# Kernel optimization log

Measured on AMD Instinct MI355X. Metric: run time of the kernel, lower is better.

Reference implementation:

```python
import jax, jax.numpy as jnp
import numpy as np

N_WAY = 2
K_SHOT = 5
C = 320
NPTS = 2048
NQ = 2
K_PROTO = 100  # hardcoded k=100 in forward
N_CLS = N_WAY + 1
SIGMA = 1.0
NEG = -1e9


def _l2norm(x, eps=1e-8):
    return x / (jnp.linalg.norm(x, axis=-1, keepdims=True) + eps)


def _class_prototypes(feat, mask, k):
    """Multi-prototype masked pooling for one class.
    feat: [M, C] point features; mask: [M] float (1 = belongs to class).
    Picks k masked seed points, assigns every masked point to its
    nearest (cosine) seed, and returns the k masked cluster means.
    """
    M = feat.shape[0]
    # deterministic seeds: first k masked points (tie-break by index)
    score = mask - jnp.arange(M, dtype=feat.dtype) * 1e-9
    _, seed_idx = jax.lax.top_k(score, k)
    seeds = feat[seed_idx]                      # [k, C]
    sim = _l2norm(feat) @ _l2norm(seeds).T      # [M, k]
    assign = jnp.argmax(sim, axis=1)            # [M]
    onehot = jax.nn.one_hot(assign, k, dtype=feat.dtype) * mask[:, None]  # [M, k]
    num = onehot.T @ feat                       # [k, C]
    den = onehot.sum(axis=0)[:, None] + 1e-8
    return num / den


def _fg_prototypes(support_feat, fg_mask, k):
    # support_feat [n_way, k_shot, C, N] -> per-class point sets [n_way, k_shot*N, C]
    feat = support_feat.transpose(0, 1, 3, 2).reshape(N_WAY, -1, C)
    m = fg_mask.reshape(N_WAY, -1).astype(feat.dtype)
    protos = jax.vmap(lambda f, mm: _class_prototypes(f, mm, k))(feat, m)  # [n_way, k, C]
    labels = jnp.repeat(jnp.arange(1, N_WAY + 1), k)                        # classes 1..n_way
    return protos.reshape(-1, C), jax.nn.one_hot(labels, N_CLS, dtype=feat.dtype)


def _bg_prototypes(support_feat, bg_mask, k):
    feat = support_feat.transpose(0, 1, 3, 2).reshape(-1, C)   # all shots pooled
    m = bg_mask.reshape(-1).astype(feat.dtype)
    protos = _class_prototypes(feat, m, k)                      # [k, C]
    labels = jnp.zeros((k,), dtype=jnp.int32)                   # class 0 = background
    return protos, jax.nn.one_hot(labels, N_CLS, dtype=feat.dtype)


def _predict(prototypes, proto_onehot, qfeat, qlabels):
    # cosine similarity [M, P], per-class max over that class's prototypes
    sim = (_l2norm(qfeat) @ _l2norm(prototypes).T) / SIGMA        # [M, P]
    cls_mask = proto_onehot.T[None] > 0                            # [1, ncls, P]
    pred = jnp.max(jnp.where(cls_mask, sim[:, None, :], NEG), axis=-1)  # [M, ncls]
    logp = jax.nn.log_softmax(pred, axis=-1)
    loss = -jnp.mean(jnp.take_along_axis(logp, qlabels.reshape(-1, 1), axis=1))
    query_pred = pred.reshape(NQ, NPTS, N_CLS).transpose(0, 2, 1)  # [NQ, ncls, NPTS]
    return loss, query_pred


def reference(support_feat, query_feat, support_y, query_y):
    fg_mask = support_y
    bg_mask = 1 - support_y
    fg_protos, fg_labels = _fg_prototypes(support_feat, fg_mask, K_PROTO)
    bg_protos, bg_labels = _bg_prototypes(support_feat, bg_mask, K_PROTO)
    prototypes = jnp.concatenate([bg_protos, fg_protos], axis=0)           # [P, C]
    proto_labels = jnp.concatenate([bg_labels, fg_labels], axis=0)         # [P, ncls]

    qfeat = query_feat.transpose(0, 2, 1).reshape(-1, C)                   # [NQ*NPTS, C]
    loss, query_pred = _predict(prototypes, proto_labels, qfeat, query_y)
    # the forward adds computeCrossEntropyLoss(query_pred, query_y): same CE again
    loss = loss * 2.0

    # post-hoc per-point confidence thresholding (vectorized Python loop)
    qp = jnp.concatenate([query_pred[0], query_pred[1]], axis=-1)          # [ncls, NQ*NPTS]
    predictions = jnp.argmax(qp, axis=0)
    confidences = jnp.max(qp, axis=0)
    final = jnp.where(confidences > jnp.mean(confidences), predictions, -1)
    final_labels = jnp.stack([final[:NPTS], final[NPTS:]], axis=0)         # [2, NPTS]
    return loss, query_pred, final_labels


def setup_inputs() -> dict:
    key = jax.random.key(0)
    k1, k2, k3, k4 = jax.random.split(key, 4)
    return {
        "support_feat": jax.random.normal(k1, (N_WAY, K_SHOT, C, NPTS), dtype=jnp.float32),
        "query_feat": jax.random.normal(k2, (NQ, C, NPTS), dtype=jnp.float32),
        "support_y": jax.random.randint(k3, (N_WAY, K_SHOT, NPTS), 0, 2, dtype=jnp.int32),
        "query_y": jax.random.randint(k4, (NQ, NPTS), 0, 3, dtype=jnp.int32),
    }
```

## Files before the change

### kernel.cpp

```cpp
#include <hip/hip_runtime.h>
#include <math.h>

#define C 320
#define NPTS 2048
#define SUPPTS 20480
#define QPTS 4096
#define KP 100
#define NCLS 3
#define PSTRIDE 300

__global__ __launch_bounds__(64) void k_protoseed(const float* __restrict__ sup,
                                                  const int* __restrict__ sy,
                                                  float* __restrict__ pbufT) {
    int p    = blockIdx.x;
    int lane = threadIdx.x;
    int prob = (p < 100) ? 2 : ((p < 200) ? 0 : 1);
    int rank = (p < 100) ? p : ((p < 200) ? p - 100 : p - 200);
    int M    = (prob == 2) ? SUPPTS : 10240;
    int base = (prob == 1) ? 10240 : 0;
    int found = 0, sp = 0;
    for (int chunk = 0; chunk < M; chunk += 64) {
        int yy = sy[base + chunk + lane];
        int m  = (prob == 2) ? (1 - yy) : yy;
        unsigned long long bal = __ballot(m != 0);
        int cnt = __popcll(bal);
        if (found + cnt > rank) {
            int need = rank - found;
            int prefix = __popcll(bal & ((1ull << lane) - 1ull));
            unsigned long long match = __ballot(m && (prefix == need));
            int pos = __ffsll((unsigned long long)match) - 1;
            sp = base + chunk + pos;
            break;
        }
        found += cnt;
    }
    const float* fb = sup + ((size_t)(sp >> 11) * C) * NPTS + (sp & 2047);
    float v[5]; float s = 0.f;
    #pragma unroll
    for (int i = 0; i < 5; i++) {
        v[i] = fb[(size_t)(lane + i * 64) * NPTS];
        s += v[i] * v[i];
    }
    #pragma unroll
    for (int off = 32; off > 0; off >>= 1) s += __shfl_down(s, off);
    s = __shfl(s, 0);
    float r = 1.0f / (sqrtf(s) + 1e-8f);
    #pragma unroll
    for (int i = 0; i < 5; i++)
        pbufT[(size_t)(lane + i * 64) * PSTRIDE + p] = v[i] * r;
}

__global__ __launch_bounds__(128) void k_assign(const float* __restrict__ sup,
                                                const float* __restrict__ pbT,
                                                float* __restrict__ pmaxv,
                                                int* __restrict__ pmaxj) {
    __shared__ float shp[C * 20];
    int b = blockIdx.x, jt = blockIdx.y, tid = threadIdx.x;
    int prob, pt, gbase, aoff;
    if (b < 40)       { prob = 0; pt = b * 256;         gbase = 0;     aoff = 0; }
    else if (b < 80)  { prob = 1; pt = (b - 40) * 256;  gbase = 10240; aoff = 10240; }
    else              { prob = 2; pt = (b - 80) * 256;  gbase = 0;     aoff = 20480; }
    int j0 = jt * 20;
    int col0 = (prob == 2) ? 0 : (100 + prob * 100);
    for (int i = tid; i < C * 20; i += 128) {
        int j = i % 20, c = i / 20;
        shp[i] = pbT[(size_t)c * PSTRIDE + col0 + j0 + j];
    }
    __syncthreads();
    int g = gbase + pt + tid * 2;
    const float* fb = sup + ((size_t)(g >> 11) * C) * NPTS + (g & 2047);
    float acc0[20], acc1[20];
    #pragma unroll
    for (int j = 0; j < 20; j++) { acc0[j] = 0.f; acc1[j] = 0.f; }
    float2 pf[8];
    #pragma unroll
    for (int k = 0; k < 8; k++) pf[k] = *(const float2*)(fb + (size_t)k * NPTS);
    for (int cc = 0; cc < C; cc += 8) {
        float2 cur[8];
        #pragma unroll
        for (int k = 0; k < 8; k++) cur[k] = pf[k];
        if (cc + 8 < C) {
            #pragma unroll
            for (int k = 0; k < 8; k++) pf[k] = *(const float2*)(fb + (size_t)(cc + 8 + k) * NPTS);
        }
        #pragma unroll
        for (int k = 0; k < 8; k++) {
            const float4* r = (const float4*)&shp[(cc + k) * 20];
            float4 a = r[0], d1 = r[1], d2 = r[2], d3 = r[3], d4 = r[4];
            float px = cur[k].x, py = cur[k].y;
            acc0[0]+=px*a.x;  acc1[0]+=py*a.x;  acc0[1]+=px*a.y;  acc1[1]+=py*a.y;
            acc0[2]+=px*a.z;  acc1[2]+=py*a.z;  acc0[3]+=px*a.w;  acc1[3]+=py*a.w;
            acc0[4]+=px*d1.x; acc1[4]+=py*d1.x; acc0[5]+=px*d1.y; acc1[5]+=py*d1.y;
            acc0[6]+=px*d1.z; acc1[6]+=py*d1.z; acc0[7]+=px*d1.w; acc1[7]+=py*d1.w;
            acc0[8]+=px*d2.x; acc1[8]+=py*d2.x; acc0[9]+=px*d2.y; acc1[9]+=py*d2.y;
            acc0[10]+=px*d2.z;acc1[10]+=py*d2.z;acc0[11]+=px*d2.w;acc1[11]+=py*d2.w;
            acc0[12]+=px*d3.x;acc1[12]+=py*d3.x;acc0[13]+=px*d3.y;acc1[13]+=py*d3.y;
            acc0[14]+=px*d3.z;acc1[14]+=py*d3.z;acc0[15]+=px*d3.w;acc1[15]+=py*d3.w;
            acc0[16]+=px*d4.x;acc1[16]+=py*d4.x;acc0[17]+=px*d4.y;acc1[17]+=py*d4.y;
            acc0[18]+=px*d4.z;acc1[18]+=py*d4.z;acc0[19]+=px*d4.w;acc1[19]+=py*d4.w;
        }
    }
    float bv0 = acc0[0]; int bj0 = 0;
    float bv1 = acc1[0]; int bj1 = 0;
    #pragma unroll
    for (int j = 1; j < 20; j++) {
        if (acc0[j] > bv0) { bv0 = acc0[j]; bj0 = j; }
        if (acc1[j] > bv1) { bv1 = acc1[j]; bj1 = j; }
    }
    size_t a0 = (size_t)jt * 40960 + (aoff + pt + tid * 2);
    pmaxv[a0]     = bv0; pmaxj[a0]     = j0 + bj0;
    pmaxv[a0 + 1] = bv1; pmaxj[a0 + 1] = j0 + bj1;
}

__global__ __launch_bounds__(256) void k_combine_dst(const float* __restrict__ pmaxv,
                                                     const int* __restrict__ pmaxj,
                                                     const int* __restrict__ sy,
                                                     int* __restrict__ dst,
                                                     float* __restrict__ loss) {
    int g = blockIdx.x * 256 + threadIdx.x;
    if (g == 0) loss[0] = 0.f;
    if (g == 1) loss[1] = 0.f;
    float bvf = pmaxv[g]; int bjf = pmaxj[g];
    #pragma unroll
    for (int t = 1; t < 5; t++) {
        float v = pmaxv[(size_t)t * 40960 + g];
        if (v > bvf) { bvf = v; bjf = pmaxj[(size_t)t * 40960 + g]; }
    }
    float bvb = pmaxv[SUPPTS + g]; int bjb = pmaxj[SUPPTS + g];
    #pragma unroll
    for (int t = 1; t < 5; t++) {
        float v = pmaxv[(size_t)t * 40960 + SUPPTS + g];
        if (v > bvb) { bvb = v; bjb = pmaxj[(size_t)t * 40960 + SUPPTS + g]; }
    }
    int way = (g >= 10240) ? 1 : 0;
    dst[g] = sy[g] ? (100 + way * 100 + bjf) : bjb;
}

__global__ __launch_bounds__(256) void k_accum_lds(const float* __restrict__ sup,
                                                   const int* __restrict__ dst,
                                                   float* __restrict__ part,
                                                   float* __restrict__ cnt) {
    __shared__ float bins[8 * 800];
    __shared__ float scnt[800];
    int bx = blockIdx.x;
    int ct = blockIdx.y;
    int tid = threadIdx.x;
    int copy = tid & 3;
    int ws = bx >> 1, half = bx & 1;
    int w = (ws >= 5) ? 1 : 0;
    int nbase = half * 1024;
    for (int i = tid; i < 8 * 800; i += 256) bins[i] = 0.f;
    if (ct == 0) { for (int i = tid; i < 800; i += 256) scnt[i] = 0.f; }
    int dreg[4];
    #pragma unroll
    for (int sub = 0; sub < 4; sub++) {
        int d = dst[ws * 2048 + nbase + sub * 256 + tid];
        dreg[sub] = (d < 100) ? d : (d - w * 100);
    }
    __syncthreads();
    if (ct == 0) {
        #pragma unroll
        for (int sub = 0; sub < 4; sub++) atomicAdd(&scnt[copy * 200 + dreg[sub]], 1.0f);
    }
    const float* base = sup + ((size_t)ws * C + ct * 8) * NPTS + nbase;
    for (int cl = 0; cl < 8; cl++) {
        const float* row = base + (size_t)cl * NPTS;
        #pragma unroll
        for (int sub = 0; sub < 4; sub++)
            atomicAdd(&bins[cl * 800 + copy * 200 + dreg[sub]], row[sub * 256 + tid]);
    }
    __syncthreads();
    float* pout = part + (size_t)(bx * 40 + ct) * 1600;
    for (int i = tid; i < 8 * 200; i += 256) {
        int bin = i >> 3, cl = i & 7;
        float s = bins[cl * 800 + bin] + bins[cl * 800 + 200 + bin]
                + bins[cl * 800 + 400 + bin] + bins[cl * 800 + 600 + bin];
        pout[i] = s;
    }
    if (ct == 0 && tid < 200)
        cnt[bx * 200 + tid] = scnt[tid] + scnt[200 + tid] + scnt[400 + tid] + scnt[600 + tid];
}

__global__ __launch_bounds__(64) void k_reduce_proto(const float* __restrict__ part,
                                                     const float* __restrict__ cnt,
                                                     float* __restrict__ phatT) {
    int d   = blockIdx.x;
    int tid = threadIdx.x;
    int local, s0, ns;
    if (d < 100)      { local = d;       s0 = 0;  ns = 20; }
    else if (d < 200) { local = d;       s0 = 0;  ns = 10; }
    else              { local = d - 100; s0 = 10; ns = 10; }
    float dn = 0.f;
    for (int k = 0; k < ns; k++) dn += cnt[(s0 + k) * 200 + local];
    float inv = 1.0f / (dn + 1e-8f);
    float vals[5]; float sq = 0.f;
    #pragma unroll
    for (int i = 0; i < 5; i++) {
        int c = tid + i * 64;
        int ct = c >> 3, cl = c & 7;
        float s = 0.f;
        for (int k = 0; k < ns; k++)
            s += part[(size_t)((s0 + k) * 40 + ct) * 1600 + local * 8 + cl];
        float v = s * inv;
        vals[i] = v; sq += v * v;
    }
    #pragma unroll
    for (int off = 32; off > 0; off >>= 1) sq += __shfl_down(sq, off);
    sq = __shfl(sq, 0);
    float rn = 1.0f / (sqrtf(sq) + 1e-8f);
    #pragma unroll
    for (int i = 0; i < 5; i++)
        phatT[(size_t)(tid + i * 64) * PSTRIDE + d] = vals[i] * rn;
}

__global__ __launch_bounds__(256) void k_qpartial(const float* __restrict__ qry,
                                                  const float* __restrict__ phT,
                                                  float* __restrict__ qmaxv,
                                                  float* __restrict__ qrn) {
    __shared__ float shp[C * 16];
    __shared__ float red[3 * 64 * 45];
    int pb = blockIdx.x, jt = blockIdx.y, tid = threadIdx.x;
    int wave = tid >> 6, lane = tid & 63;
    int j0 = jt * 10;
    for (int i = tid; i < C * 10; i += 256) {
        int j = i % 10, c = i / 10;
        shp[c * 16 + j] = phT[(size_t)c * PSTRIDE + j0 + j];
    }
    __syncthreads();
    int m = pb * 256 + lane * 4;
    int c0 = wave * 80;
    const float* fb = qry + ((size_t)(m >> 11) * C + c0) * NPTS + (m & 2047);
    float acc[4][10];
    #pragma unroll
    for (int p = 0; p < 4; p++)
        #pragma unroll
        for (int j = 0; j < 10; j++) acc[p][j] = 0.f;
    float qn[4] = {0.f, 0.f, 0.f, 0.f};
    float4 pf[8];
    #pragma unroll
    for (int k = 0; k < 8; k++) pf[k] = *(const float4*)(fb + (size_t)k * NPTS);
    for (int cc = 0; cc < 80; cc += 8) {
        float4 cur[8];
        #pragma unroll
        for (int k = 0; k < 8; k++) cur[k] = pf[k];
        if (cc + 8 < 80) {
            #pragma unroll
            for (int k = 0; k < 8; k++) pf[k] = *(const float4*)(fb + (size_t)(cc + 8 + k) * NPTS);
        }
        #pragma unroll
        for (int k = 0; k < 8; k++) {
            const float* row = &shp[(c0 + cc + k) * 16];
            float4 p0 = ((const float4*)row)[0];
            float4 p1 = ((const float4*)row)[1];
            float2 p2 = ((const float2*)row)[4];
            float pr[10] = {p0.x,p0.y,p0.z,p0.w,p1.x,p1.y,p1.z,p1.w,p2.x,p2.y};
            float4 cv = cur[k];
            if (jt == 0) {
                qn[0] += cv.x*cv.x; qn[1] += cv.y*cv.y; qn[2] += cv.z*cv.z; qn[3] += cv.w*cv.w;
            }
            #pragma unroll
            for (int j = 0; j < 10; j++) {
                acc[0][j] += cv.x * pr[j];
                acc[1][j] += cv.y * pr[j];
                acc[2][j] += cv.z * pr[j];
                acc[3][j] += cv.w * pr[j];
            }
        }
    }
    if (wave > 0) {
        float* my = red + ((wave - 1) * 64 + lane) * 45;
        #pragma unroll
        for (int p = 0; p < 4; p++)
            #pragma unroll
            for (int j = 0; j < 10; j++) my[p * 10 + j] = acc[p][j];
        #pragma unroll
        for (int p = 0; p < 4; p++) my[40 + p] = qn[p];
    }
    __syncthreads();
    if (wave == 0) {
        #pragma unroll
        for (int w = 0; w < 3; w++) {
            const float* my = red + (w * 64 + lane) * 45;
            #pragma unroll
            for (int p = 0; p < 4; p++)
                #pragma unroll
                for (int j = 0; j < 10; j++) acc[p][j] += my[p * 10 + j];
            #pragma unroll
            for (int p = 0; p < 4; p++) qn[p] += my[40 + p];
        }
        #pragma unroll
        for (int p = 0; p < 4; p++) {
            float bv = acc[p][0];
            #pragma unroll
            for (int j = 1; j < 10; j++) bv = fmaxf(bv, acc[p][j]);
            qmaxv[(size_t)(m + p) * 30 + jt] = bv;
        }
        if (jt == 0) {
            #pragma unroll
            for (int p = 0; p < 4; p++) qrn[m + p] = 1.0f / (sqrtf(qn[p]) + 1e-8f);
        }
    }
}

__global__ __launch_bounds__(256) void k_pred(const float* __restrict__ qmaxv,
                                              const float* __restrict__ qrn,
                                              const int* __restrict__ qy,
                                              float* __restrict__ out,
                                              float* __restrict__ lossacc,
                                              float* __restrict__ cbuf,
                                              int* __restrict__ lbuf) {
    __shared__ float redL[256];
    __shared__ float redC[256];
    int tid = threadIdx.x;
    int m = blockIdx.x * 256 + tid;
    float rn = qrn[m];
    float pred[NCLS];
    #pragma unroll
    for (int cls = 0; cls < NCLS; cls++) {
        float g = qmaxv[(size_t)m * 30 + cls * 10];
        #pragma unroll
        for (int t = 1; t < 10; t++) g = fmaxf(g, qmaxv[(size_t)m * 30 + cls * 10 + t]);
        pred[cls] = rn * g;
    }
    int q = m >> 11, n = m & 2047;
    #pragma unroll
    for (int cls = 0; cls < NCLS; cls++)
        out[1 + ((size_t)(q * NCLS + cls)) * NPTS + n] = pred[cls];
    float mx = fmaxf(pred[0], fmaxf(pred[1], pred[2]));
    float lse = mx + logf(expf(pred[0] - mx) + expf(pred[1] - mx) + expf(pred[2] - mx));
    int lab = 0; float cf = pred[0];
    if (pred[1] > cf) { cf = pred[1]; lab = 1; }
    if (pred[2] > cf) { cf = pred[2]; lab = 2; }
    cbuf[m] = cf; lbuf[m] = lab;
    redL[tid] = lse - pred[qy[m]];
    redC[tid] = cf;
    __syncthreads();
    for (int off = 128; off > 0; off >>= 1) {
        if (tid < off) { redL[tid] += redL[tid + off]; redC[tid] += redC[tid + off]; }
        __syncthreads();
    }
    if (tid == 0) {
        atomicAdd(&lossacc[0], redL[0]);
        atomicAdd(&lossacc[1], redC[0]);
    }
}

__global__ __launch_bounds__(256) void k_final(const float* __restrict__ cbuf,
                                               const int* __restrict__ lbuf,
                                               const float* __restrict__ lossacc,
                                               float* __restrict__ out) {
    int m = blockIdx.x * 256 + threadIdx.x;
    float mean = lossacc[1] / (float)QPTS;
    float cf = cbuf[m];
    out[1 + 2 * NCLS * NPTS + m] = (cf > mean) ? (float)lbuf[m] : -1.0f;
    if (m == 0) out[0] = 2.0f * lossacc[0] / (float)QPTS;
}

extern "C" void kernel_launch(void* const* d_in, const int* in_sizes, int n_in,
                              void* d_out, int out_size, void* d_ws, size_t ws_size,
                              hipStream_t stream) {
    const float* sup = (const float*)d_in[0];
    const float* qry = (const float*)d_in[1];
    const int*   sy  = (const int*)d_in[2];
    const int*   qy  = (const int*)d_in[3];
    float* out = (float*)d_out;

    float* f      = (float*)d_ws;
    float* qrn    = f;
    float* cnt    = qrn + QPTS;
    float* pbufT  = cnt + 4000;
    float* phatT  = pbufT + 96000;
    float* loss   = phatT + 96000;
    int*   dstb   = (int*)(loss + 4);
    float* trans  = (float*)(dstb + SUPPTS);
    float* pmaxv  = trans;
    int*   pmaxj  = (int*)(pmaxv + 204800);
    float* part   = trans;
    float* qmaxv  = trans;
    float* cbuf   = qmaxv + 122880;
    int*   lbuf   = (int*)(cbuf + QPTS);

    k_protoseed<<<300, 64, 0, stream>>>(sup, sy, pbufT);
    {
        dim3 grid(160, 5);
        k_assign<<<grid, 128, 0, stream>>>(sup, pbufT, pmaxv, pmaxj);
    }
    k_combine_dst<<<80, 256, 0, stream>>>(pmaxv, pmaxj, sy, dstb, loss);
    {
        dim3 grid(20, 40);
        k_accum_lds<<<grid, 256, 0, stream>>>(sup, dstb, part, cnt);
    }
    k_reduce_proto<<<300, 64, 0, stream>>>(part, cnt, phatT);
    {
        dim3 grid(16, 30);
        k_qpartial<<<grid, 256, 0, stream>>>(qry, phatT, qmaxv, qrn);
    }
    k_pred<<<16, 256, 0, stream>>>(qmaxv, qrn, qy, out, loss, cbuf, lbuf);
    k_final<<<16, 256, 0, stream>>>(cbuf, lbuf, loss, out);
}
```

Measured before the change: 237.0 us.

## Fuse all stages into one persistent kernel with software grid barriers

Replaces the eight separate kernel launches with a single 400-block persistent kernel that runs each stage in turn, separated by atomic-counter grid barriers, with the barrier counters cleared by a memset before launch. The goal is to remove per-launch overhead and inter-kernel gaps. The per-stage work splits also change: k_assign now covers 512 points per block, and the query pass no longer splits channels across waves. This relies on all 400 blocks being co-resident; if they are not, the spin barrier can hang or time out and give wrong results. The barrier spins and the idle blocks in the small stages add cost of their own.

```diff
diff --git a/kernel.cpp b/kernel.cpp
--- a/kernel.cpp
+++ b/kernel.cpp
@@ -8,285 +8,297 @@
 #define KP 100
 #define NCLS 3
 #define PSTRIDE 300
-
-__global__ __launch_bounds__(64) void k_protoseed(const float* __restrict__ sup,
-                                                  const int* __restrict__ sy,
-                                                  float* __restrict__ pbufT) {
-    int p    = blockIdx.x;
-    int lane = threadIdx.x;
-    int prob = (p < 100) ? 2 : ((p < 200) ? 0 : 1);
-    int rank = (p < 100) ? p : ((p < 200) ? p - 100 : p - 200);
-    int M    = (prob == 2) ? SUPPTS : 10240;
-    int base = (prob == 1) ? 10240 : 0;
-    int found = 0, sp = 0;
-    for (int chunk = 0; chunk < M; chunk += 64) {
-        int yy = sy[base + chunk + lane];
-        int m  = (prob == 2) ? (1 - yy) : yy;
-        unsigned long long bal = __ballot(m != 0);
-        int cnt = __popcll(bal);
-        if (found + cnt > rank) {
-            int need = rank - found;
-            int prefix = __popcll(bal & ((1ull << lane) - 1ull));
-            unsigned long long match = __ballot(m && (prefix == need));
-            int pos = __ffsll((unsigned long long)match) - 1;
-            sp = base + chunk + pos;
-            break;
-        }
-        found += cnt;
-    }
-    const float* fb = sup + ((size_t)(sp >> 11) * C) * NPTS + (sp & 2047);
-    float v[5]; float s = 0.f;
-    #pragma unroll
-    for (int i = 0; i < 5; i++) {
-        v[i] = fb[(size_t)(lane + i * 64) * NPTS];
-        s += v[i] * v[i];
-    }
-    #pragma unroll
-    for (int off = 32; off > 0; off >>= 1) s += __shfl_down(s, off);
-    s = __shfl(s, 0);
-    float r = 1.0f / (sqrtf(s) + 1e-8f);
-    #pragma unroll
-    for (int i = 0; i < 5; i++)
-        pbufT[(size_t)(lane + i * 64) * PSTRIDE + p] = v[i] * r;
+#define NB 400
+
+__device__ __forceinline__ void gridbar(int* bar, int idx) {
+    __syncthreads();
+    if (threadIdx.x == 0) {
+        __threadfence();
+        atomicAdd(&bar[idx], 1);
+        long spins = 0;
+        while (atomicAdd(&bar[idx], 0) < NB) {
+            if (++spins > (1L << 27)) break;
+        }
+        __threadfence();
+    }
+    __syncthreads();
 }
 
-__global__ __launch_bounds__(128) void k_assign(const float* __restrict__ sup,
-                                                const float* __restrict__ pbT,
-                                                float* __restrict__ pmaxv,
-                                                int* __restrict__ pmaxj) {
-    __shared__ float shp[C * 20];
-    int b = blockIdx.x, jt = blockIdx.y, tid = threadIdx.x;
-    int prob, pt, gbase, aoff;
-    if (b < 40)       { prob = 0; pt = b * 256;         gbase = 0;     aoff = 0; }
-    else if (b < 80)  { prob = 1; pt = (b - 40) * 256;  gbase = 10240; aoff = 10240; }
-    else              { prob = 2; pt = (b - 80) * 256;  gbase = 0;     aoff = 20480; }
-    int j0 = jt * 20;
-    int col0 = (prob == 2) ? 0 : (100 + prob * 100);
-    for (int i = tid; i < C * 20; i += 128) {
-        int j = i % 20, c = i / 20;
-        shp[i] = pbT[(size_t)c * PSTRIDE + col0 + j0 + j];
-    }
-    __syncthreads();
-    int g = gbase + pt + tid * 2;
-    const float* fb = sup + ((size_t)(g >> 11) * C) * NPTS + (g & 2047);
-    float acc0[20], acc1[20];
-    #pragma unroll
-    for (int j = 0; j < 20; j++) { acc0[j] = 0.f; acc1[j] = 0.f; }
-    float2 pf[8];
-    #pragma unroll
-    for (int k = 0; k < 8; k++) pf[k] = *(const float2*)(fb + (size_t)k * NPTS);
-    for (int cc = 0; cc < C; cc += 8) {
-        float2 cur[8];
-        #pragma unroll
-        for (int k = 0; k < 8; k++) cur[k] = pf[k];
-        if (cc + 8 < C) {
-            #pragma unroll
-            for (int k = 0; k < 8; k++) pf[k] = *(const float2*)(fb + (size_t)(cc + 8 + k) * NPTS);
-        }
-        #pragma unroll
-        for (int k = 0; k < 8; k++) {
-            const float4* r = (const float4*)&shp[(cc + k) * 20];
-            float4 a = r[0], d1 = r[1], d2 = r[2], d3 = r[3], d4 = r[4];
-            float px = cur[k].x, py = cur[k].y;
-            acc0[0]+=px*a.x;  acc1[0]+=py*a.x;  acc0[1]+=px*a.y;  acc1[1]+=py*a.y;
-            acc0[2]+=px*a.z;  acc1[2]+=py*a.z;  acc0[3]+=px*a.w;  acc1[3]+=py*a.w;
-            acc0[4]+=px*d1.x; acc1[4]+=py*d1.x; acc0[5]+=px*d1.y; acc1[5]+=py*d1.y;
-            acc0[6]+=px*d1.z; acc1[6]+=py*d1.z; acc0[7]+=px*d1.w; acc1[7]+=py*d1.w;
-            acc0[8]+=px*d2.x; acc1[8]+=py*d2.x; acc0[9]+=px*d2.y; acc1[9]+=py*d2.y;
-            acc0[10]+=px*d2.z;acc1[10]+=py*d2.z;acc0[11]+=px*d2.w;acc1[11]+=py*d2.w;
-            acc0[12]+=px*d3.x;acc1[12]+=py*d3.x;acc0[13]+=px*d3.y;acc1[13]+=py*d3.y;
-            acc0[14]+=px*d3.z;acc1[14]+=py*d3.z;acc0[15]+=px*d3.w;acc1[15]+=py*d3.w;
-            acc0[16]+=px*d4.x;acc1[16]+=py*d4.x;acc0[17]+=px*d4.y;acc1[17]+=py*d4.y;
-            acc0[18]+=px*d4.z;acc1[18]+=py*d4.z;acc0[19]+=px*d4.w;acc1[19]+=py*d4.w;
-        }
-    }
-    float bv0 = acc0[0]; int bj0 = 0;
-    float bv1 = acc1[0]; int bj1 = 0;
-    #pragma unroll
-    for (int j = 1; j < 20; j++) {
-        if (acc0[j] > bv0) { bv0 = acc0[j]; bj0 = j; }
-        if (acc1[j] > bv1) { bv1 = acc1[j]; bj1 = j; }
-    }
-    size_t a0 = (size_t)jt * 40960 + (aoff + pt + tid * 2);
-    pmaxv[a0]     = bv0; pmaxj[a0]     = j0 + bj0;
-    pmaxv[a0 + 1] = bv1; pmaxj[a0 + 1] = j0 + bj1;
-}
-
-__global__ __launch_bounds__(256) void k_combine_dst(const float* __restrict__ pmaxv,
-                                                     const int* __restrict__ pmaxj,
-                                                     const int* __restrict__ sy,
-                                                     int* __restrict__ dst,
-                                                     float* __restrict__ loss) {
-    int g = blockIdx.x * 256 + threadIdx.x;
-    if (g == 0) loss[0] = 0.f;
-    if (g == 1) loss[1] = 0.f;
-    float bvf = pmaxv[g]; int bjf = pmaxj[g];
-    #pragma unroll
-    for (int t = 1; t < 5; t++) {
-        float v = pmaxv[(size_t)t * 40960 + g];
-        if (v > bvf) { bvf = v; bjf = pmaxj[(size_t)t * 40960 + g]; }
-    }
-    float bvb = pmaxv[SUPPTS + g]; int bjb = pmaxj[SUPPTS + g];
-    #pragma unroll
-    for (int t = 1; t < 5; t++) {
-        float v = pmaxv[(size_t)t * 40960 + SUPPTS + g];
-        if (v > bvb) { bvb = v; bjb = pmaxj[(size_t)t * 40960 + SUPPTS + g]; }
-    }
-    int way = (g >= 10240) ? 1 : 0;
-    dst[g] = sy[g] ? (100 + way * 100 + bjf) : bjb;
-}
-
-__global__ __launch_bounds__(256) void k_accum_lds(const float* __restrict__ sup,
-                                                   const int* __restrict__ dst,
-                                                   float* __restrict__ part,
-                                                   float* __restrict__ cnt) {
-    __shared__ float bins[8 * 800];
-    __shared__ float scnt[800];
-    int bx = blockIdx.x;
-    int ct = blockIdx.y;
-    int tid = threadIdx.x;
-    int copy = tid & 3;
-    int ws = bx >> 1, half = bx & 1;
-    int w = (ws >= 5) ? 1 : 0;
-    int nbase = half * 1024;
-    for (int i = tid; i < 8 * 800; i += 256) bins[i] = 0.f;
-    if (ct == 0) { for (int i = tid; i < 800; i += 256) scnt[i] = 0.f; }
-    int dreg[4];
-    #pragma unroll
-    for (int sub = 0; sub < 4; sub++) {
-        int d = dst[ws * 2048 + nbase + sub * 256 + tid];
-        dreg[sub] = (d < 100) ? d : (d - w * 100);
-    }
-    __syncthreads();
-    if (ct == 0) {
-        #pragma unroll
-        for (int sub = 0; sub < 4; sub++) atomicAdd(&scnt[copy * 200 + dreg[sub]], 1.0f);
-    }
-    const float* base = sup + ((size_t)ws * C + ct * 8) * NPTS + nbase;
-    for (int cl = 0; cl < 8; cl++) {
-        const float* row = base + (size_t)cl * NPTS;
-        #pragma unroll
-        for (int sub = 0; sub < 4; sub++)
-            atomicAdd(&bins[cl * 800 + copy * 200 + dreg[sub]], row[sub * 256 + tid]);
-    }
-    __syncthreads();
-    float* pout = part + (size_t)(bx * 40 + ct) * 1600;
-    for (int i = tid; i < 8 * 200; i += 256) {
-        int bin = i >> 3, cl = i & 7;
-        float s = bins[cl * 800 + bin] + bins[cl * 800 + 200 + bin]
-                + bins[cl * 800 + 400 + bin] + bins[cl * 800 + 600 + bin];
-        pout[i] = s;
-    }
-    if (ct == 0 && tid < 200)
-        cnt[bx * 200 + tid] = scnt[tid] + scnt[200 + tid] + scnt[400 + tid] + scnt[600 + tid];
-}
-
-__global__ __launch_bounds__(64) void k_reduce_proto(const float* __restrict__ part,
-                                                     const float* __restrict__ cnt,
-                                                     float* __restrict__ phatT) {
-    int d   = blockIdx.x;
-    int tid = threadIdx.x;
-    int local, s0, ns;
-    if (d < 100)      { local = d;       s0 = 0;  ns = 20; }
-    else if (d < 200) { local = d;       s0 = 0;  ns = 10; }
-    else              { local = d - 100; s0 = 10; ns = 10; }
-    float dn = 0.f;
-    for (int k = 0; k < ns; k++) dn += cnt[(s0 + k) * 200 + local];
-    float inv = 1.0f / (dn + 1e-8f);
-    float vals[5]; float sq = 0.f;
-    #pragma unroll
-    for (int i = 0; i < 5; i++) {
-        int c = tid + i * 64;
-        int ct = c >> 3, cl = c & 7;
-        float s = 0.f;
-        for (int k = 0; k < ns; k++)
-            s += part[(size_t)((s0 + k) * 40 + ct) * 1600 + local * 8 + cl];
-        float v = s * inv;
-        vals[i] = v; sq += v * v;
-    }
-    #pragma unroll
-    for (int off = 32; off > 0; off >>= 1) sq += __shfl_down(sq, off);
-    sq = __shfl(sq, 0);
-    float rn = 1.0f / (sqrtf(sq) + 1e-8f);
-    #pragma unroll
-    for (int i = 0; i < 5; i++)
-        phatT[(size_t)(tid + i * 64) * PSTRIDE + d] = vals[i] * rn;
-}
-
-__global__ __launch_bounds__(256) void k_qpartial(const float* __restrict__ qry,
-                                                  const float* __restrict__ phT,
-                                                  float* __restrict__ qmaxv,
-                                                  float* __restrict__ qrn) {
-    __shared__ float shp[C * 16];
-    __shared__ float red[3 * 64 * 45];
-    int pb = blockIdx.x, jt = blockIdx.y, tid = threadIdx.x;
-    int wave = tid >> 6, lane = tid & 63;
-    int j0 = jt * 10;
-    for (int i = tid; i < C * 10; i += 256) {
-        int j = i % 10, c = i / 10;
-        shp[c * 16 + j] = phT[(size_t)c * PSTRIDE + j0 + j];
-    }
-    __syncthreads();
-    int m = pb * 256 + lane * 4;
-    int c0 = wave * 80;
-    const float* fb = qry + ((size_t)(m >> 11) * C + c0) * NPTS + (m & 2047);
-    float acc[4][10];
-    #pragma unroll
-    for (int p = 0; p < 4; p++)
-        #pragma unroll
-        for (int j = 0; j < 10; j++) acc[p][j] = 0.f;
-    float qn[4] = {0.f, 0.f, 0.f, 0.f};
-    float4 pf[8];
-    #pragma unroll
-    for (int k = 0; k < 8; k++) pf[k] = *(const float4*)(fb + (size_t)k * NPTS);
-    for (int cc = 0; cc < 80; cc += 8) {
-        float4 cur[8];
-        #pragma unroll
-        for (int k = 0; k < 8; k++) cur[k] = pf[k];
-        if (cc + 8 < 80) {
-            #pragma unroll
-            for (int k = 0; k < 8; k++) pf[k] = *(const float4*)(fb + (size_t)(cc + 8 + k) * NPTS);
-        }
-        #pragma unroll
-        for (int k = 0; k < 8; k++) {
-            const float* row = &shp[(c0 + cc + k) * 16];
-            float4 p0 = ((const float4*)row)[0];
-            float4 p1 = ((const float4*)row)[1];
-            float2 p2 = ((const float2*)row)[4];
-            float pr[10] = {p0.x,p0.y,p0.z,p0.w,p1.x,p1.y,p1.z,p1.w,p2.x,p2.y};
-            float4 cv = cur[k];
-            if (jt == 0) {
-                qn[0] += cv.x*cv.x; qn[1] += cv.y*cv.y; qn[2] += cv.z*cv.z; qn[3] += cv.w*cv.w;
-            }
-            #pragma unroll
-            for (int j = 0; j < 10; j++) {
-                acc[0][j] += cv.x * pr[j];
-                acc[1][j] += cv.y * pr[j];
-                acc[2][j] += cv.z * pr[j];
-                acc[3][j] += cv.w * pr[j];
-            }
-        }
-    }
-    if (wave > 0) {
-        float* my = red + ((wave - 1) * 64 + lane) * 45;
+__global__ __launch_bounds__(256, 2) void k_mega(const float* __restrict__ sup,
+                                                 const float* __restrict__ qry,
+                                                 const int* __restrict__ sy,
+                                                 const int* __restrict__ qy,
+                                                 float* __restrict__ out,
+                                                 float* __restrict__ wsf) {
+    float* qrn   = wsf;
+    float* cnt   = qrn + QPTS;
+    float* pbufT = cnt + 4000;
+    float* phatT = pbufT + 96000;
+    float* loss  = phatT + 96000;
+    int*   bar   = (int*)(loss + 4);
+    int*   dstb  = bar + 8;
+    float* trans = (float*)(dstb + SUPPTS);
+    float* pmaxv = trans;
+    int*   pmaxj = (int*)(pmaxv + 204800);
+    float* part  = trans;
+    float* qmaxv = trans;
+    float* cbuf  = qmaxv + 122880;
+    int*   lbuf  = (int*)(cbuf + QPTS);
+
+    __shared__ __align__(16) float smem[7200];
+
+    int bid = blockIdx.x, tid = threadIdx.x;
+
+    {
+        int w = bid * 4 + (tid >> 6);
+        int lane = tid & 63;
+        if (w < 300) {
+            int p = w;
+            int prob = (p < 100) ? 2 : ((p < 200) ? 0 : 1);
+            int rank = (p < 100) ? p : ((p < 200) ? p - 100 : p - 200);
+            int M    = (prob == 2) ? SUPPTS : 10240;
+            int base = (prob == 1) ? 10240 : 0;
+            int found = 0, sp = 0;
+            for (int chunk = 0; chunk < M; chunk += 64) {
+                int yy = sy[base + chunk + lane];
+                int m  = (prob == 2) ? (1 - yy) : yy;
+                unsigned long long bal = __ballot(m != 0);
+                int cb = __popcll(bal);
+                if (found + cb > rank) {
+                    int need = rank - found;
+                    int prefix = __popcll(bal & ((1ull << lane) - 1ull));
+                    unsigned long long match = __ballot(m && (prefix == need));
+                    int pos = __ffsll(match) - 1;
+                    sp = base + chunk + pos;
+                    break;
+                }
+                found += cb;
+            }
+            const float* fb = sup + ((size_t)(sp >> 11) * C) * NPTS + (sp & 2047);
+            float v[5]; float s = 0.f;
+            #pragma unroll
+            for (int i = 0; i < 5; i++) {
+                v[i] = fb[(size_t)(lane + i * 64) * NPTS];
+                s += v[i] * v[i];
+            }
+            #pragma unroll
+            for (int off = 32; off > 0; off >>= 1) s += __shfl_down(s, off);
+            s = __shfl(s, 0);
+            float r = 1.0f / (sqrtf(s) + 1e-8f);
+            #pragma unroll
+            for (int i = 0; i < 5; i++)
+                pbufT[(size_t)(lane + i * 64) * PSTRIDE + p] = v[i] * r;
+        }
+    }
+    gridbar(bar, 0);
+
+    {
+        float* shp = smem;
+        int b2 = bid % 80, jt = bid / 80;
+        int prob, pt, gbase, aoff;
+        if (b2 < 20)      { prob = 0; pt = b2 * 512;        gbase = 0;     aoff = 0; }
+        else if (b2 < 40) { prob = 1; pt = (b2 - 20) * 512; gbase = 10240; aoff = 10240; }
+        else              { prob = 2; pt = (b2 - 40) * 512; gbase = 0;     aoff = 20480; }
+        int j0 = jt * 20;
+        int col0 = (prob == 2) ? 0 : (100 + prob * 100);
+        for (int i = tid; i < C * 20; i += 256) {
+            int j = i % 20, c = i / 20;
+            shp[i] = pbufT[(size_t)c * PSTRIDE + col0 + j0 + j];
+        }
+        __syncthreads();
+        int g = gbase + pt + tid * 2;
+        const float* fb = sup + ((size_t)(g >> 11) * C) * NPTS + (g & 2047);
+        float acc0[20], acc1[20];
+        #pragma unroll
+        for (int j = 0; j < 20; j++) { acc0[j] = 0.f; acc1[j] = 0.f; }
+        float2 pf[8];
+        #pragma unroll
+        for (int k = 0; k < 8; k++) pf[k] = *(const float2*)(fb + (size_t)k * NPTS);
+        for (int cc = 0; cc < C; cc += 8) {
+            float2 cur[8];
+            #pragma unroll
+            for (int k = 0; k < 8; k++) cur[k] = pf[k];
+            if (cc + 8 < C) {
+                #pragma unroll
+                for (int k = 0; k < 8; k++) pf[k] = *(const float2*)(fb + (size_t)(cc + 8 + k) * NPTS);
+            }
+            #pragma unroll
+            for (int k = 0; k < 8; k++) {
+                const float4* r = (const float4*)&shp[(cc + k) * 20];
+                float4 a = r[0], d1 = r[1], d2 = r[2], d3 = r[3], d4 = r[4];
+                float px = cur[k].x, py = cur[k].y;
+                acc0[0]+=px*a.x;  acc1[0]+=py*a.x;  acc0[1]+=px*a.y;  acc1[1]+=py*a.y;
+                acc0[2]+=px*a.z;  acc1[2]+=py*a.z;  acc0[3]+=px*a.w;  acc1[3]+=py*a.w;
+                acc0[4]+=px*d1.x; acc1[4]+=py*d1.x; acc0[5]+=px*d1.y; acc1[5]+=py*d1.y;
+                acc0[6]+=px*d1.z; acc1[6]+=py*d1.z; acc0[7]+=px*d1.w; acc1[7]+=py*d1.w;
+                acc0[8]+=px*d2.x; acc1[8]+=py*d2.x; acc0[9]+=px*d2.y; acc1[9]+=py*d2.y;
+                acc0[10]+=px*d2.z;acc1[10]+=py*d2.z;acc0[11]+=px*d2.w;acc1[11]+=py*d2.w;
+                acc0[12]+=px*d3.x;acc1[12]+=py*d3.x;acc0[13]+=px*d3.y;acc1[13]+=py*d3.y;
+                acc0[14]+=px*d3.z;acc1[14]+=py*d3.z;acc0[15]+=px*d3.w;acc1[15]+=py*d3.w;
+                acc0[16]+=px*d4.x;acc1[16]+=py*d4.x;acc0[17]+=px*d4.y;acc1[17]+=py*d4.y;
+                acc0[18]+=px*d4.z;acc1[18]+=py*d4.z;acc0[19]+=px*d4.w;acc1[19]+=py*d4.w;
+            }
+        }
+        float bv0 = acc0[0]; int bj0 = 0;
+        float bv1 = acc1[0]; int bj1 = 0;
+        #pragma unroll
+        for (int j = 1; j < 20; j++) {
+            if (acc0[j] > bv0) { bv0 = acc0[j]; bj0 = j; }
+            if (acc1[j] > bv1) { bv1 = acc1[j]; bj1 = j; }
+        }
+        size_t a0 = (size_t)jt * 40960 + (aoff + pt + tid * 2);
+        pmaxv[a0]     = bv0; pmaxj[a0]     = j0 + bj0;
+        pmaxv[a0 + 1] = bv1; pmaxj[a0 + 1] = j0 + bj1;
+    }
+    gridbar(bar, 1);
+
+    if (bid < 80) {
+        int g = bid * 256 + tid;
+        if (g == 0) loss[0] = 0.f;
+        if (g == 1) loss[1] = 0.f;
+        float bvf = pmaxv[g]; int bjf = pmaxj[g];
+        #pragma unroll
+        for (int t = 1; t < 5; t++) {
+            float v = pmaxv[(size_t)t * 40960 + g];
+            if (v > bvf) { bvf = v; bjf = pmaxj[(size_t)t * 40960 + g]; }
+        }
+        float bvb = pmaxv[SUPPTS + g]; int bjb = pmaxj[SUPPTS + g];
+        #pragma unroll
+        for (int t = 1; t < 5; t++) {
+            float v = pmaxv[(size_t)t * 40960 + SUPPTS + g];
+            if (v > bvb) { bvb = v; bjb = pmaxj[(size_t)t * 40960 + SUPPTS + g]; }
+        }
+        int way = (g >= 10240) ? 1 : 0;
+        dstb[g] = sy[g] ? (100 + way * 100 + bjf) : bjb;
+    }
+    gridbar(bar, 2);
+
+    {
+        float* bins = smem;
+        float* scnt = smem + 6400;
+        int copy = tid & 3;
+        for (int v = bid; v < 800; v += NB) {
+            int bx = v % 20, ct = v / 20;
+            int ws = bx >> 1, half = bx & 1;
+            int w = (ws >= 5) ? 1 : 0;
+            int nbase = half * 1024;
+            for (int i = tid; i < 8 * 800; i += 256) bins[i] = 0.f;
+            if (ct == 0) { for (int i = tid; i < 800; i += 256) scnt[i] = 0.f; }
+            int dreg[4];
+            #pragma unroll
+            for (int sub = 0; sub < 4; sub++) {
+                int d = dstb[ws * 2048 + nbase + sub * 256 + tid];
+                dreg[sub] = (d < 100) ? d : (d - w * 100);
+            }
+            __syncthreads();
+            if (ct == 0) {
+                #pragma unroll
+                for (int sub = 0; sub < 4; sub++) atomicAdd(&scnt[copy * 200 + dreg[sub]], 1.0f);
+            }
+            const float* base = sup + ((size_t)ws * C + ct * 8) * NPTS + nbase;
+            for (int cl = 0; cl < 8; cl++) {
+                const float* row = base + (size_t)cl * NPTS;
+                #pragma unroll
+                for (int sub = 0; sub < 4; sub++)
+                    atomicAdd(&bins[cl * 800 + copy * 200 + dreg[sub]], row[sub * 256 + tid]);
+            }
+            __syncthreads();
+            float* pout = part + (size_t)(bx * 40 + ct) * 1600;
+            for (int i = tid; i < 8 * 200; i += 256) {
+                int bin = i >> 3, cl = i & 7;
+                pout[i] = bins[cl * 800 + bin] + bins[cl * 800 + 200 + bin]
+                        + bins[cl * 800 + 400 + bin] + bins[cl * 800 + 600 + bin];
+            }
+            if (ct == 0 && tid < 200)
+                cnt[bx * 200 + tid] = scnt[tid] + scnt[200 + tid] + scnt[400 + tid] + scnt[600 + tid];
+            __syncthreads();
+        }
+    }
+    gridbar(bar, 3);
+
+    {
+        int w = bid * 4 + (tid >> 6);
+        int lane = tid & 63;
+        if (w < 300) {
+            int d = w;
+            int local, s0, ns;
+            if (d < 100)      { local = d;       s0 = 0;  ns = 20; }
+            else if (d < 200) { local = d;       s0 = 0;  ns = 10; }
+            else              { local = d - 100; s0 = 10; ns = 10; }
+            float dn = 0.f;
+            for (int k = 0; k < ns; k++) dn += cnt[(s0 + k) * 200 + local];
+            float inv = 1.0f / (dn + 1e-8f);
+            float vals[5]; float sq = 0.f;
+            #pragma unroll
+            for (int i = 0; i < 5; i++) {
+                int c = lane + i * 64;
+                int ct = c >> 3, cl = c & 7;
+                float s = 0.f;
+                for (int k = 0; k < ns; k++)
+                    s += part[(size_t)((s0 + k) * 40 + ct) * 1600 + local * 8 + cl];
+                float v = s * inv;
+                vals[i] = v; sq += v * v;
+            }
+            #pragma unroll
+            for (int off = 32; off > 0; off >>= 1) sq += __shfl_down(sq, off);
+            sq = __shfl(sq, 0);
+            float rn = 1.0f / (sqrtf(sq) + 1e-8f);
+            #pragma unroll
+            for (int i = 0; i < 5; i++)
+                phatT[(size_t)(lane + i * 64) * PSTRIDE + d] = vals[i] * rn;
+        }
+    }
+    gridbar(bar, 4);
+
+    if (bid < 120) {
+        float* shp = smem;
+        int jt = bid % 30;
+        int pb = (bid / 30) * 4 + (tid >> 6);
+        int lane = tid & 63;
+        int j0 = jt * 10;
+        for (int i = tid; i < C * 10; i += 256) {
+            int j = i % 10, c = i / 10;
+            shp[c * 16 + j] = phatT[(size_t)c * PSTRIDE + j0 + j];
+        }
+        __syncthreads();
+        int m = pb * 256 + lane * 4;
+        const float* fb = qry + ((size_t)(m >> 11) * C) * NPTS + (m & 2047);
+        float acc[4][10];
         #pragma unroll
         for (int p = 0; p < 4; p++)
             #pragma unroll
-            for (int j = 0; j < 10; j++) my[p * 10 + j] = acc[p][j];
-        #pragma unroll
-        for (int p = 0; p < 4; p++) my[40 + p] = qn[p];
-    }
-    __syncthreads();
-    if (wave == 0) {
-        #pragma unroll
-        for (int w = 0; w < 3; w++) {
-            const float* my = red + (w * 64 + lane) * 45;
-            #pragma unroll
-            for (int p = 0; p < 4; p++)
-                #pragma unroll
-                for (int j = 0; j < 10; j++) acc[p][j] += my[p * 10 + j];
-            #pragma unroll
-            for (int p = 0; p < 4; p++) qn[p] += my[40 + p];
+            for (int j = 0; j < 10; j++) acc[p][j] = 0.f;
+        float qn[4] = {0.f, 0.f, 0.f, 0.f};
+        float4 pf[8];
+        #pragma unroll
+        for (int k = 0; k < 8; k++) pf[k] = *(const float4*)(fb + (size_t)k * NPTS);
+        for (int cc = 0; cc < C; cc += 8) {
+            float4 cur[8];
+            #pragma unroll
+            for (int k = 0; k < 8; k++) cur[k] = pf[k];
+            if (cc + 8 < C) {
+                #pragma unroll
+                for (int k = 0; k < 8; k++) pf[k] = *(const float4*)(fb + (size_t)(cc + 8 + k) * NPTS);
+            }
+            #pragma unroll
+            for (int k = 0; k < 8; k++) {
+                const float* row = &shp[(cc + k) * 16];
+                float4 p0 = ((const float4*)row)[0];
+                float4 p1 = ((const float4*)row)[1];
+                float2 p2 = ((const float2*)row)[4];
+                float pr[10] = {p0.x,p0.y,p0.z,p0.w,p1.x,p1.y,p1.z,p1.w,p2.x,p2.y};
+                float4 cv = cur[k];
+                if (jt == 0) {
+                    qn[0] += cv.x*cv.x; qn[1] += cv.y*cv.y; qn[2] += cv.z*cv.z; qn[3] += cv.w*cv.w;
+                }
+                #pragma unroll
+                for (int j = 0; j < 10; j++) {
+                    acc[0][j] += cv.x * pr[j];
+                    acc[1][j] += cv.y * pr[j];
+                    acc[2][j] += cv.z * pr[j];
+                    acc[3][j] += cv.w * pr[j];
+                }
+            }
         }
         #pragma unroll
         for (int p = 0; p < 4; p++) {
@@ -300,60 +312,52 @@
             for (int p = 0; p < 4; p++) qrn[m + p] = 1.0f / (sqrtf(qn[p]) + 1e-8f);
         }
     }
-}
-
-__global__ __launch_bounds__(256) void k_pred(const float* __restrict__ qmaxv,
-                                              const float* __restrict__ qrn,
-                                              const int* __restrict__ qy,
-                                              float* __restrict__ out,
-                                              float* __restrict__ lossacc,
-                                              float* __restrict__ cbuf,
-                                              int* __restrict__ lbuf) {
-    __shared__ float redL[256];
-    __shared__ float redC[256];
-    int tid = threadIdx.x;
-    int m = blockIdx.x * 256 + tid;
-    float rn = qrn[m];
-    float pred[NCLS];
-    #pragma unroll
-    for (int cls = 0; cls < NCLS; cls++) {
-        float g = qmaxv[(size_t)m * 30 + cls * 10];
-        #pragma unroll
-        for (int t = 1; t < 10; t++) g = fmaxf(g, qmaxv[(size_t)m * 30 + cls * 10 + t]);
-        pred[cls] = rn * g;
-    }
-    int q = m >> 11, n = m & 2047;
-    #pragma unroll
-    for (int cls = 0; cls < NCLS; cls++)
-        out[1 + ((size_t)(q * NCLS + cls)) * NPTS + n] = pred[cls];
-    float mx = fmaxf(pred[0], fmaxf(pred[1], pred[2]));
-    float lse = mx + logf(expf(pred[0] - mx) + expf(pred[1] - mx) + expf(pred[2] - mx));
-    int lab = 0; float cf = pred[0];
-    if (pred[1] > cf) { cf = pred[1]; lab = 1; }
-    if (pred[2] > cf) { cf = pred[2]; lab = 2; }
-    cbuf[m] = cf; lbuf[m] = lab;
-    redL[tid] = lse - pred[qy[m]];
-    redC[tid] = cf;
-    __syncthreads();
-    for (int off = 128; off > 0; off >>= 1) {
-        if (tid < off) { redL[tid] += redL[tid + off]; redC[tid] += redC[tid + off]; }
+    gridbar(bar, 5);
+
+    if (bid < 16) {
+        float* redL = smem;
+        float* redC = smem + 256;
+        int m = bid * 256 + tid;
+        float rn = qrn[m];
+        float pred[NCLS];
+        #pragma unroll
+        for (int cls = 0; cls < NCLS; cls++) {
+            float g = qmaxv[(size_t)m * 30 + cls * 10];
+            #pragma unroll
+            for (int t = 1; t < 10; t++) g = fmaxf(g, qmaxv[(size_t)m * 30 + cls * 10 + t]);
+            pred[cls] = rn * g;
+        }
+        int q = m >> 11, n = m & 2047;
+        #pragma unroll
+        for (int cls = 0; cls < NCLS; cls++)
+            out[1 + ((size_t)(q * NCLS + cls)) * NPTS + n] = pred[cls];
+        float mx = fmaxf(pred[0], fmaxf(pred[1], pred[2]));
+        float lse = mx + logf(expf(pred[0] - mx) + expf(pred[1] - mx) + expf(pred[2] - mx));
+        int lab = 0; float cf = pred[0];
+        if (pred[1] > cf) { cf = pred[1]; lab = 1; }
+        if (pred[2] > cf) { cf = pred[2]; lab = 2; }
+        cbuf[m] = cf; lbuf[m] = lab;
+        redL[tid] = lse - pred[qy[m]];
+        redC[tid] = cf;
         __syncthreads();
-    }
-    if (tid == 0) {
-        atomicAdd(&lossacc[0], redL[0]);
-        atomicAdd(&lossacc[1], redC[0]);
-    }
-}
-
-__global__ __launch_bounds__(256) void k_final(const float* __restrict__ cbuf,
-                                               const int* __restrict__ lbuf,
-                                               const float* __restrict__ lossacc,
-                                               float* __restrict__ out) {
-    int m = blockIdx.x * 256 + threadIdx.x;
-    float mean = lossacc[1] / (float)QPTS;
-    float cf = cbuf[m];
-    out[1 + 2 * NCLS * NPTS + m] = (cf > mean) ? (float)lbuf[m] : -1.0f;
-    if (m == 0) out[0] = 2.0f * lossacc[0] / (float)QPTS;
+        for (int off = 128; off > 0; off >>= 1) {
+            if (tid < off) { redL[tid] += redL[tid + off]; redC[tid] += redC[tid + off]; }
+            __syncthreads();
+        }
+        if (tid == 0) {
+            atomicAdd(&loss[0], redL[0]);
+            atomicAdd(&loss[1], redC[0]);
+        }
+    }
+    gridbar(bar, 6);
+
+    if (bid < 16) {
+        int m = bid * 256 + tid;
+        float mean = loss[1] / (float)QPTS;
+        float cf = cbuf[m];
+        out[1 + 2 * NCLS * NPTS + m] = (cf > mean) ? (float)lbuf[m] : -1.0f;
+        if (m == 0) out[0] = 2.0f * loss[0] / (float)QPTS;
+    }
 }
 
 extern "C" void kernel_launch(void* const* d_in, const int* in_sizes, int n_in,
@@ -364,37 +368,10 @@
     const int*   sy  = (const int*)d_in[2];
     const int*   qy  = (const int*)d_in[3];
     float* out = (float*)d_out;
-
-    float* f      = (float*)d_ws;
-    float* qrn    = f;
-    float* cnt    = qrn + QPTS;
-    float* pbufT  = cnt + 4000;
-    float* phatT  = pbufT + 96000;
-    float* loss   = phatT + 96000;
-    int*   dstb   = (int*)(loss + 4);
-    float* trans  = (float*)(dstb + SUPPTS);
-    float* pmaxv  = trans;
-    int*   pmaxj  = (int*)(pmaxv + 204800);
-    float* part   = trans;
-    float* qmaxv  = trans;
-    float* cbuf   = qmaxv + 122880;
-    int*   lbuf   = (int*)(cbuf + QPTS);
-
-    k_protoseed<<<300, 64, 0, stream>>>(sup, sy, pbufT);
-    {
-        dim3 grid(160, 5);
-        k_assign<<<grid, 128, 0, stream>>>(sup, pbufT, pmaxv, pmaxj);
-    }
-    k_combine_dst<<<80, 256, 0, stream>>>(pmaxv, pmaxj, sy, dstb, loss);
-    {
-        dim3 grid(20, 40);
-        k_accum_lds<<<grid, 256, 0, stream>>>(sup, dstb, part, cnt);
-    }
-    k_reduce_proto<<<300, 64, 0, stream>>>(part, cnt, phatT);
-    {
-        dim3 grid(16, 30);
-        k_qpartial<<<grid, 256, 0, stream>>>(qry, phatT, qmaxv, qrn);
-    }
-    k_pred<<<16, 256, 0, stream>>>(qmaxv, qrn, qy, out, loss, cbuf, lbuf);
-    k_final<<<16, 256, 0, stream>>>(cbuf, lbuf, loss, out);
+    float* wsf = (float*)d_ws;
+
+    int* bar = (int*)(wsf + QPTS + 4000 + 96000 + 96000 + 4);
+    hipMemsetAsync(bar, 0, 8 * sizeof(int), stream);
+
+    k_mega<<<NB, 256, 0, stream>>>(sup, qry, sy, qy, out, wsf);
 }
```

Result: slower. 497.2 us (+109.8%).
